# Optimization experiments

Measured on AMD Instinct MI355X. Metric: run time of the kernel, lower is better.

Reference implementation:

```python
import jax, jax.numpy as jnp
import numpy as np

B, I, H = 512, 256, 512
UNFOLDS = 6


def setup_inputs() -> dict:
    key = jax.random.key(0)
    ks = jax.random.split(key, 13)
    u = lambda k, shape, lo, hi: jax.random.uniform(k, shape, jnp.float32, lo, hi)
    sensory_erev = (2.0 * jax.random.randint(ks[3], (I, H), 0, 2) - 1.0).astype(jnp.float32)
    erev = (2.0 * jax.random.randint(ks[7], (H, H), 0, 2) - 1.0).astype(jnp.float32)
    return {
        "inputs": jax.random.normal(ks[0], (B, I), jnp.float32),
        "state": jax.random.normal(ks[1], (B, H), jnp.float32),
        "sensory_mu": u(ks[2], (I, H), 0.3, 0.8),
        "sensory_sigma": u(ks[4], (I, H), 3.0, 8.0),
        "sensory_W": u(ks[5], (I, H), 0.01, 1.0),
        "sensory_erev": sensory_erev,
        "mu": u(ks[6], (H, H), 0.3, 0.8),
        "sigma": u(ks[8], (H, H), 3.0, 8.0),
        "W": u(ks[9], (H, H), 0.01, 1.0),
        "erev": erev,
        "vleak": u(ks[10], (H,), -0.2, 0.2),
        "gleak": jnp.ones((H,), jnp.float32),
        "cm": jnp.full((H,), 0.5, jnp.float32),
    }


def reference(inputs, state, sensory_mu, sensory_sigma, sensory_W, sensory_erev,
              mu, sigma, W, erev, vleak, gleak, cm):
    # Sensory synapse currents (computed once): (B, I, H) broadcast
    sensory_act = jax.nn.sigmoid((inputs[:, :, None] - sensory_mu[None]) * sensory_sigma[None])
    sensory_w_act = sensory_W[None] * sensory_act                      # (B, I, H)
    w_num_sensory = jnp.sum(sensory_w_act * sensory_erev[None], axis=1)  # (B, H)
    w_den_sensory = jnp.sum(sensory_w_act, axis=1)                        # (B, H)

    def step(v_pre, _):
        # recurrent synapse gating: (B, H_pre, H_post)
        act = jax.nn.sigmoid((v_pre[:, :, None] - mu[None]) * sigma[None])
        w_act = W[None] * act
        w_num = jnp.sum(w_act * erev[None], axis=1) + w_num_sensory
        w_den = jnp.sum(w_act, axis=1) + w_den_sensory
        numerator = cm * v_pre + gleak * vleak + w_num
        denominator = cm + gleak + w_den
        return numerator / (denominator + 1e-8), None

    v_pre, _ = jax.lax.scan(step, state, None, length=UNFOLDS)
    return v_pre
```

## Files before the change

kernel.cpp:

```cpp
#include <hip/hip_runtime.h>

#define LTC_B 512
#define LTC_H 512
#define LTC_I 256

static constexpr float kL2E = 1.4426950408889634f;

struct alignas(16) HPair { _Float16 a0, a1, c0, c1, wz0, wz1, wd0, wd1; };

typedef unsigned int u32;
#define AS_G __attribute__((address_space(1)))
#define AS_L __attribute__((address_space(3)))

__device__ __forceinline__ void ldg_lds16(const void* g, void* l) {
    __builtin_amdgcn_global_load_lds((const AS_G u32*)g, (AS_L u32*)l, 16, 0, 0);
}

template<int K>
__global__ void ltc_prep(const float* __restrict__ mu, const float* __restrict__ sigma,
                         const float* __restrict__ W, const float* __restrict__ erev,
                         HPair* __restrict__ slab) {
    const int t = blockIdx.x * 256 + threadIdx.x;
    if (t >= K * 256) return;
    const int hh   = t & 63;
    const int rest = t >> 6;
    const int jp   = rest & (K / 2 - 1);
    const int ht   = rest / (K / 2);
    const int h    = ht * 64 + hh;
    const int g0   = (2 * jp) * LTC_H + h;
    const int g1   = g0 + LTC_H;
    HPair o;
    o.a0 = (_Float16)(-sigma[g0] * kL2E);
    o.a1 = (_Float16)(-sigma[g1] * kL2E);
    o.c0 = (_Float16)(mu[g0] * sigma[g0] * kL2E);
    o.c1 = (_Float16)(mu[g1] * sigma[g1] * kL2E);
    o.wz0 = (_Float16)(W[g0] * erev[g0]);
    o.wz1 = (_Float16)(W[g1] * erev[g1]);
    o.wd0 = (_Float16)(W[g0]);
    o.wd1 = (_Float16)(W[g1]);
    slab[t] = o;
}

template<int K, bool RECUR>
__global__ __launch_bounds__(256, 4)
void ltc_pass(const float* __restrict__ vsrc,
              const HPair* __restrict__ slab,
              const float* __restrict__ snum, const float* __restrict__ sden,
              const float* __restrict__ vleak, const float* __restrict__ gleak,
              const float* __restrict__ cm,
              float* __restrict__ onum, float* __restrict__ oden,
              float* __restrict__ vout)
{
    __shared__ HPair wbuf[2][16 * 64];
    const int tid  = threadIdx.x;
    const int lane = tid & 63;
    const int wu   = __builtin_amdgcn_readfirstlane(tid >> 6);
    const int ht   = blockIdx.x;
    const int b    = blockIdx.y * 4 + wu;
    const float* __restrict__ vrow = vsrc + (size_t)b * K;

    constexpr int NC = K / 32;
    const int rot = (int)((blockIdx.x + 7u * blockIdx.y) & (NC - 1));
    const char* slabt = (const char*)slab + (size_t)ht * (K * 512);

    {
        const char* src = slabt + rot * 16384 + wu * 4096;
        char* dst = (char*)&wbuf[0][0] + wu * 4096;
        #pragma unroll
        for (int rr = 0; rr < 4; ++rr)
            ldg_lds16(src + rr * 1024 + lane * 16, dst + rr * 1024);
    }

    float na = 0.f, da = 0.f;

    #pragma unroll
    for (int i = 0; i < NC; ++i) {
        const int c = (rot + i) & (NC - 1);
        __syncthreads();
        if (i + 1 < NC) {
            const int cn = (rot + i + 1) & (NC - 1);
            const char* src = slabt + cn * 16384 + wu * 4096;
            char* dst = (char*)&wbuf[(i + 1) & 1][0] + wu * 4096;
            #pragma unroll
            for (int rr = 0; rr < 4; ++rr)
                ldg_lds16(src + rr * 1024 + lane * 16, dst + rr * 1024);
        }
        const HPair* wb = &wbuf[i & 1][0];
        const float* __restrict__ vch = vrow + c * 32;

        HPair pr[16];
        #pragma unroll
        for (int jj = 0; jj < 16; ++jj) pr[jj] = wb[jj * 64 + lane];

        #pragma unroll
        for (int jj = 0; jj < 16; ++jj) {
            const float vj0 = vch[2 * jj];
            const float vj1 = vch[2 * jj + 1];
            const float t0 = fmaf((float)pr[jj].a0, vj0, (float)pr[jj].c0);
            const float t1 = fmaf((float)pr[jj].a1, vj1, (float)pr[jj].c1);
            const float e0 = __builtin_amdgcn_exp2f(t0);
            const float e1 = __builtin_amdgcn_exp2f(t1);
            const float d0 = 1.0f + e0;
            const float d1 = 1.0f + e1;
            const float rr = __builtin_amdgcn_rcpf(d0 * d1);
            const float s0 = rr * d1;
            const float s1 = rr * d0;
            na = fmaf((float)pr[jj].wz0, s0, na);
            da = fmaf((float)pr[jj].wd0, s0, da);
            na = fmaf((float)pr[jj].wz1, s1, na);
            da = fmaf((float)pr[jj].wd1, s1, da);
        }
    }

    const int h  = ht * 64 + lane;
    const int bh = b * LTC_H + h;
    if constexpr (RECUR) {
        const float gl = gleak[h], vl = vleak[h], c0 = cm[h];
        const float vp = vsrc[bh];
        const float num = fmaf(c0, vp, gl * vl) + na + snum[bh];
        const float den = c0 + gl + da + sden[bh];
        vout[bh] = num * __builtin_amdgcn_rcpf(den + 1e-8f);
    } else {
        onum[bh] = na;
        oden[bh] = da;
    }
}

extern "C" void kernel_launch(void* const* d_in, const int* in_sizes, int n_in,
                              void* d_out, int out_size, void* d_ws, size_t ws_size,
                              hipStream_t stream) {
    const float* inputs = (const float*)d_in[0];
    const float* state  = (const float*)d_in[1];
    const float* smu    = (const float*)d_in[2];
    const float* ssig   = (const float*)d_in[3];
    const float* sW     = (const float*)d_in[4];
    const float* serev  = (const float*)d_in[5];
    const float* mu     = (const float*)d_in[6];
    const float* sig    = (const float*)d_in[7];
    const float* W      = (const float*)d_in[8];
    const float* erev   = (const float*)d_in[9];
    const float* vleak  = (const float*)d_in[10];
    const float* gleak  = (const float*)d_in[11];
    const float* cm     = (const float*)d_in[12];

    float* out  = (float*)d_out;
    char*  ws   = (char*)d_ws;
    float* snum = (float*)(ws);
    float* sden = (float*)(ws + 1 * 1048576);
    float* vA   = (float*)(ws + 2 * 1048576);
    HPair* rslab = (HPair*)(ws + 3 * 1048576);
    HPair* sslab = (HPair*)(ws + 5 * 1048576);

    ltc_prep<LTC_H><<<LTC_H * 256 / 256, 256, 0, stream>>>(mu, sig, W, erev, rslab);
    ltc_prep<LTC_I><<<LTC_I * 256 / 256, 256, 0, stream>>>(smu, ssig, sW, serev, sslab);

    dim3 grid(LTC_H / 64, LTC_B / 4);
    dim3 blk(256);

    ltc_pass<LTC_I, false><<<grid, blk, 0, stream>>>(
        inputs, sslab, nullptr, nullptr, nullptr, nullptr, nullptr,
        snum, sden, nullptr);

    const float* vin = state;
    float* targets[6] = {vA, out, vA, out, vA, out};
    for (int s = 0; s < 6; ++s) {
        ltc_pass<LTC_H, true><<<grid, blk, 0, stream>>>(
            vin, rslab, snum, sden, vleak, gleak, cm,
            nullptr, nullptr, targets[s]);
        vin = targets[s];
    }
}
```

Before: 333.3 us.

## Transpose state to H-major, fp32 precomputed slab, split K across waves

```diff
diff --git a/kernel.cpp b/kernel.cpp
--- a/kernel.cpp
+++ b/kernel.cpp
@@ -6,123 +6,120 @@
 
 static constexpr float kL2E = 1.4426950408889634f;
 
-struct alignas(16) HPair { _Float16 a0, a1, c0, c1, wz0, wz1, wd0, wd1; };
-
-typedef unsigned int u32;
-#define AS_G __attribute__((address_space(1)))
-#define AS_L __attribute__((address_space(3)))
-
-__device__ __forceinline__ void ldg_lds16(const void* g, void* l) {
-    __builtin_amdgcn_global_load_lds((const AS_G u32*)g, (AS_L u32*)l, 16, 0, 0);
-}
-
-template<int K>
+template<int K, int LOG2K>
 __global__ void ltc_prep(const float* __restrict__ mu, const float* __restrict__ sigma,
                          const float* __restrict__ W, const float* __restrict__ erev,
-                         HPair* __restrict__ slab) {
+                         float4* __restrict__ slab) {
     const int t = blockIdx.x * 256 + threadIdx.x;
-    if (t >= K * 256) return;
-    const int hh   = t & 63;
-    const int rest = t >> 6;
-    const int jp   = rest & (K / 2 - 1);
-    const int ht   = rest / (K / 2);
-    const int h    = ht * 64 + hh;
-    const int g0   = (2 * jp) * LTC_H + h;
-    const int g1   = g0 + LTC_H;
-    HPair o;
-    o.a0 = (_Float16)(-sigma[g0] * kL2E);
-    o.a1 = (_Float16)(-sigma[g1] * kL2E);
-    o.c0 = (_Float16)(mu[g0] * sigma[g0] * kL2E);
-    o.c1 = (_Float16)(mu[g1] * sigma[g1] * kL2E);
-    o.wz0 = (_Float16)(W[g0] * erev[g0]);
-    o.wz1 = (_Float16)(W[g1] * erev[g1]);
-    o.wd0 = (_Float16)(W[g0]);
-    o.wd1 = (_Float16)(W[g1]);
+    if (t >= K * LTC_H) return;
+    const int hh4  = t & 3;
+    const int rest = t >> 2;
+    const int j    = rest & (K - 1);
+    const int ht4  = rest >> LOG2K;
+    const int h    = ht4 * 4 + hh4;
+    const int g    = j * LTC_H + h;
+    const float sg = sigma[g];
+    float4 o;
+    o.x = -sg * kL2E;
+    o.y = exp2f(mu[g] * sg * kL2E);
+    o.z = W[g] * erev[g];
+    o.w = W[g];
     slab[t] = o;
 }
 
-template<int K, bool RECUR>
-__global__ __launch_bounds__(256, 4)
-void ltc_pass(const float* __restrict__ vsrc,
-              const HPair* __restrict__ slab,
-              const float* __restrict__ snum, const float* __restrict__ sden,
+__global__ void ltc_transpose(const float* __restrict__ in, float* __restrict__ out,
+                              int R, int C) {
+    __shared__ float tile[64][65];
+    const int bx = blockIdx.x * 64;
+    const int by = blockIdx.y * 64;
+    const int tx = threadIdx.x & 63;
+    const int t4 = threadIdx.x >> 6;
+    #pragma unroll
+    for (int r = t4; r < 64; r += 4)
+        tile[r][tx] = in[(size_t)(by + r) * C + bx + tx];
+    __syncthreads();
+    #pragma unroll
+    for (int r = t4; r < 64; r += 4)
+        out[(size_t)(bx + r) * R + by + tx] = tile[tx][r];
+}
+
+template<int K, int MODE>
+__global__ __launch_bounds__(512, 8)
+void ltc_pass(const float* __restrict__ vT,
+              const float4* __restrict__ slab,
+              const float* __restrict__ snumT, const float* __restrict__ sdenT,
               const float* __restrict__ vleak, const float* __restrict__ gleak,
               const float* __restrict__ cm,
-              float* __restrict__ onum, float* __restrict__ oden,
-              float* __restrict__ vout)
+              float* __restrict__ o0, float* __restrict__ o1)
 {
-    __shared__ HPair wbuf[2][16 * 64];
+    constexpr int JW = K / 8;
+    __shared__ float2 comb[8][4][64];
+
     const int tid  = threadIdx.x;
     const int lane = tid & 63;
     const int wu   = __builtin_amdgcn_readfirstlane(tid >> 6);
-    const int ht   = blockIdx.x;
-    const int b    = blockIdx.y * 4 + wu;
-    const float* __restrict__ vrow = vsrc + (size_t)b * K;
+    const int ht4  = blockIdx.x;
+    const int b0   = blockIdx.y * 64;
 
-    constexpr int NC = K / 32;
-    const int rot = (int)((blockIdx.x + 7u * blockIdx.y) & (NC - 1));
-    const char* slabt = (const char*)slab + (size_t)ht * (K * 512);
+    const float4* __restrict__ wq = slab + ((size_t)ht4 * K + wu * JW) * 4;
+    const float*  __restrict__ vp = vT + (size_t)(wu * JW) * LTC_B + b0 + lane;
 
-    {
-        const char* src = slabt + rot * 16384 + wu * 4096;
-        char* dst = (char*)&wbuf[0][0] + wu * 4096;
-        #pragma unroll
-        for (int rr = 0; rr < 4; ++rr)
-            ldg_lds16(src + rr * 1024 + lane * 16, dst + rr * 1024);
+    float na0 = 0.f, da0 = 0.f, na1 = 0.f, da1 = 0.f;
+    float na2 = 0.f, da2 = 0.f, na3 = 0.f, da3 = 0.f;
+
+    #pragma unroll 4
+    for (int jj = 0; jj < JW; ++jj) {
+        const float vj = vp[(size_t)jj * LTC_B];
+        const float4 q0 = wq[jj * 4 + 0];
+        const float4 q1 = wq[jj * 4 + 1];
+        const float4 q2 = wq[jj * 4 + 2];
+        const float4 q3 = wq[jj * 4 + 3];
+        const float e0 = __builtin_amdgcn_exp2f(q0.x * vj);
+        const float e1 = __builtin_amdgcn_exp2f(q1.x * vj);
+        const float e2 = __builtin_amdgcn_exp2f(q2.x * vj);
+        const float e3 = __builtin_amdgcn_exp2f(q3.x * vj);
+        const float d0 = fmaf(q0.y, e0, 1.0f);
+        const float d1 = fmaf(q1.y, e1, 1.0f);
+        const float d2 = fmaf(q2.y, e2, 1.0f);
+        const float d3 = fmaf(q3.y, e3, 1.0f);
+        const float r01 = __builtin_amdgcn_rcpf(d0 * d1);
+        const float r23 = __builtin_amdgcn_rcpf(d2 * d3);
+        const float s0 = r01 * d1, s1 = r01 * d0;
+        const float s2 = r23 * d3, s3 = r23 * d2;
+        na0 = fmaf(q0.z, s0, na0); da0 = fmaf(q0.w, s0, da0);
+        na1 = fmaf(q1.z, s1, na1); da1 = fmaf(q1.w, s1, da1);
+        na2 = fmaf(q2.z, s2, na2); da2 = fmaf(q2.w, s2, da2);
+        na3 = fmaf(q3.z, s3, na3); da3 = fmaf(q3.w, s3, da3);
     }
 
-    float na = 0.f, da = 0.f;
+    comb[wu][0][lane] = make_float2(na0, da0);
+    comb[wu][1][lane] = make_float2(na1, da1);
+    comb[wu][2][lane] = make_float2(na2, da2);
+    comb[wu][3][lane] = make_float2(na3, da3);
+    __syncthreads();
 
-    #pragma unroll
-    for (int i = 0; i < NC; ++i) {
-        const int c = (rot + i) & (NC - 1);
-        __syncthreads();
-        if (i + 1 < NC) {
-            const int cn = (rot + i + 1) & (NC - 1);
-            const char* src = slabt + cn * 16384 + wu * 4096;
-            char* dst = (char*)&wbuf[(i + 1) & 1][0] + wu * 4096;
-            #pragma unroll
-            for (int rr = 0; rr < 4; ++rr)
-                ldg_lds16(src + rr * 1024 + lane * 16, dst + rr * 1024);
+    if (wu < 4) {
+        float na = 0.f, da = 0.f;
+        #pragma unroll
+        for (int js = 0; js < 8; ++js) {
+            const float2 p = comb[js][wu][lane];
+            na += p.x; da += p.y;
         }
-        const HPair* wb = &wbuf[i & 1][0];
-        const float* __restrict__ vch = vrow + c * 32;
-
-        HPair pr[16];
-        #pragma unroll
-        for (int jj = 0; jj < 16; ++jj) pr[jj] = wb[jj * 64 + lane];
-
-        #pragma unroll
-        for (int jj = 0; jj < 16; ++jj) {
-            const float vj0 = vch[2 * jj];
-            const float vj1 = vch[2 * jj + 1];
-            const float t0 = fmaf((float)pr[jj].a0, vj0, (float)pr[jj].c0);
-            const float t1 = fmaf((float)pr[jj].a1, vj1, (float)pr[jj].c1);
-            const float e0 = __builtin_amdgcn_exp2f(t0);
-            const float e1 = __builtin_amdgcn_exp2f(t1);
-            const float d0 = 1.0f + e0;
-            const float d1 = 1.0f + e1;
-            const float rr = __builtin_amdgcn_rcpf(d0 * d1);
-            const float s0 = rr * d1;
-            const float s1 = rr * d0;
-            na = fmaf((float)pr[jj].wz0, s0, na);
-            da = fmaf((float)pr[jj].wd0, s0, da);
-            na = fmaf((float)pr[jj].wz1, s1, na);
-            da = fmaf((float)pr[jj].wd1, s1, da);
+        const int h = ht4 * 4 + wu;
+        const int b = b0 + lane;
+        const size_t hb = (size_t)h * LTC_B + b;
+        if constexpr (MODE == 0) {
+            o0[hb] = na;
+            o1[hb] = da;
+        } else {
+            const float gl = gleak[h], vl = vleak[h], c0 = cm[h];
+            const float vpre = vT[hb];
+            const float num = fmaf(c0, vpre, gl * vl) + na + snumT[hb];
+            const float den = c0 + gl + da + sdenT[hb];
+            const float vn = num * __builtin_amdgcn_rcpf(den + 1e-8f);
+            if constexpr (MODE == 1) o0[hb] = vn;
+            else o0[(size_t)b * LTC_H + h] = vn;
         }
-    }
-
-    const int h  = ht * 64 + lane;
-    const int bh = b * LTC_H + h;
-    if constexpr (RECUR) {
-        const float gl = gleak[h], vl = vleak[h], c0 = cm[h];
-        const float vp = vsrc[bh];
-        const float num = fmaf(c0, vp, gl * vl) + na + snum[bh];
-        const float den = c0 + gl + da + sden[bh];
-        vout[bh] = num * __builtin_amdgcn_rcpf(den + 1e-8f);
-    } else {
-        onum[bh] = na;
-        oden[bh] = da;
     }
 }
 
@@ -143,30 +140,35 @@
     const float* gleak  = (const float*)d_in[11];
     const float* cm     = (const float*)d_in[12];
 
-    float* out  = (float*)d_out;
-    char*  ws   = (char*)d_ws;
-    float* snum = (float*)(ws);
-    float* sden = (float*)(ws + 1 * 1048576);
-    float* vA   = (float*)(ws + 2 * 1048576);
-    HPair* rslab = (HPair*)(ws + 3 * 1048576);
-    HPair* sslab = (HPair*)(ws + 5 * 1048576);
+    float* out = (float*)d_out;
+    char*  ws  = (char*)d_ws;
+    float*  snumT = (float*)(ws);
+    float*  sdenT = (float*)(ws + 1 * 1048576);
+    float*  vTA   = (float*)(ws + 2 * 1048576);
+    float*  vTB   = (float*)(ws + 3 * 1048576);
+    float4* rslab = (float4*)(ws + 4 * 1048576);
+    float4* sslab = (float4*)(ws + 8 * 1048576);
+    float*  inpT  = (float*)(ws + 10 * 1048576);
 
-    ltc_prep<LTC_H><<<LTC_H * 256 / 256, 256, 0, stream>>>(mu, sig, W, erev, rslab);
-    ltc_prep<LTC_I><<<LTC_I * 256 / 256, 256, 0, stream>>>(smu, ssig, sW, serev, sslab);
+    ltc_prep<LTC_H, 9><<<LTC_H * LTC_H / 256, 256, 0, stream>>>(mu, sig, W, erev, rslab);
+    ltc_prep<LTC_I, 8><<<LTC_I * LTC_H / 256, 256, 0, stream>>>(smu, ssig, sW, serev, sslab);
 
-    dim3 grid(LTC_H / 64, LTC_B / 4);
-    dim3 blk(256);
+    ltc_transpose<<<dim3(LTC_I / 64, LTC_B / 64), 256, 0, stream>>>(inputs, inpT, LTC_B, LTC_I);
+    ltc_transpose<<<dim3(LTC_H / 64, LTC_B / 64), 256, 0, stream>>>(state, vTA, LTC_B, LTC_H);
 
-    ltc_pass<LTC_I, false><<<grid, blk, 0, stream>>>(
-        inputs, sslab, nullptr, nullptr, nullptr, nullptr, nullptr,
-        snum, sden, nullptr);
+    dim3 grid(LTC_H / 4, LTC_B / 64);
+    dim3 blk(512);
 
-    const float* vin = state;
-    float* targets[6] = {vA, out, vA, out, vA, out};
-    for (int s = 0; s < 6; ++s) {
-        ltc_pass<LTC_H, true><<<grid, blk, 0, stream>>>(
-            vin, rslab, snum, sden, vleak, gleak, cm,
-            nullptr, nullptr, targets[s]);
-        vin = targets[s];
+    ltc_pass<LTC_I, 0><<<grid, blk, 0, stream>>>(
+        inpT, sslab, nullptr, nullptr, nullptr, nullptr, nullptr, snumT, sdenT);
+
+    const float* vin = vTA;
+    float* vping[5] = {vTB, vTA, vTB, vTA, vTB};
+    for (int s = 0; s < 5; ++s) {
+        ltc_pass<LTC_H, 1><<<grid, blk, 0, stream>>>(
+            vin, rslab, snumT, sdenT, vleak, gleak, cm, vping[s], nullptr);
+        vin = vping[s];
     }
+    ltc_pass<LTC_H, 2><<<grid, blk, 0, stream>>>(
+        vin, rslab, snumT, sdenT, vleak, gleak, cm, out, nullptr);
 }
```

Result: faster. 291.5 us (-12.5%).
